# Kernel optimization log

Hardware: AMD Instinct MI355X
Metric: run time of the kernel (lower is better)

Reference implementation:

```python
import jax, jax.numpy as jnp
import numpy as np

HEADS = 8
DIM_HEAD = 64
SCALE = DIM_HEAD ** -0.5
QUERY_DIM = 512
CTX_DIM = 64
INNER = HEADS * DIM_HEAD  # 512
GATE_HID = 32


def setup_inputs() -> dict:
    key = jax.random.key(0)
    ks = jax.random.split(key, 11)
    B, N, M = 4, 2048, 2048
    s = lambda fan: 1.0 / np.sqrt(fan)
    return {
        "x": jax.random.normal(ks[0], (B, N, QUERY_DIM), dtype=jnp.float32),
        "context": jax.random.normal(ks[1], (B, M, CTX_DIM), dtype=jnp.float32),
        "Wq": jax.random.normal(ks[2], (QUERY_DIM, INNER), dtype=jnp.float32) * s(QUERY_DIM),
        "Wk": jax.random.normal(ks[3], (CTX_DIM, INNER), dtype=jnp.float32) * s(CTX_DIM),
        "Wv": jax.random.normal(ks[4], (CTX_DIM, INNER), dtype=jnp.float32) * s(CTX_DIM),
        "W1": jax.random.normal(ks[5], (CTX_DIM, GATE_HID), dtype=jnp.float32) * s(CTX_DIM),
        "b1": jnp.zeros((GATE_HID,), dtype=jnp.float32),
        "W2": jax.random.normal(ks[6], (GATE_HID, 1), dtype=jnp.float32) * s(GATE_HID),
        "b2": jnp.zeros((1,), dtype=jnp.float32),
        "Wo": jax.random.normal(ks[7], (INNER, QUERY_DIM), dtype=jnp.float32) * s(INNER),
        "bo": jnp.zeros((QUERY_DIM,), dtype=jnp.float32),
    }


def reference(x, context, Wq, Wk, Wv, W1, b1, W2, b2, Wo, bo):
    B, N, _ = x.shape
    M = context.shape[1]
    # visual reliability gate: sigmoid(relu(ctx @ W1 + b1) @ W2 + b2) -> [B, M, 1]
    gate = jax.nn.sigmoid(jax.nn.relu(context @ W1 + b1) @ W2 + b2)
    ctx = context * gate
    # projections
    q = (x @ Wq).reshape(B, N, HEADS, DIM_HEAD).transpose(0, 2, 1, 3)    # [B,H,N,D]
    k = (ctx @ Wk).reshape(B, M, HEADS, DIM_HEAD).transpose(0, 2, 1, 3)  # [B,H,M,D]
    v = (ctx @ Wv).reshape(B, M, HEADS, DIM_HEAD).transpose(0, 2, 1, 3)  # [B,H,M,D]
    # scaled dot-product attention (full score matrix, as in source)
    sim = jnp.einsum('bhid,bhjd->bhij', q, k) * SCALE
    attn = jax.nn.softmax(sim, axis=-1)
    out = jnp.einsum('bhij,bhjd->bhid', attn, v)
    out = out.transpose(0, 2, 1, 3).reshape(B, N, INNER)
    return out @ Wo + bo
```

## Files before the change

kernel.cpp:

```cpp
#include <hip/hip_runtime.h>

typedef unsigned short u16;
typedef unsigned int u32;
using frag16 = __attribute__((ext_vector_type(8))) short;
using facc   = __attribute__((ext_vector_type(4))) float;
using facc16 = __attribute__((ext_vector_type(16))) float;

#define DEV static __device__ __forceinline__

DEV u16 f2bf(float f) {
  union { float f; unsigned u; } v; v.f = f;
  unsigned r = v.u + 0x7fffu + ((v.u >> 16) & 1u);
  return (u16)(r >> 16);
}
DEV unsigned fbits(float f) {
  union { float f; unsigned u; } v; v.f = f;
  return v.u;
}
DEV unsigned pkbf(float lo, float hi) {
  return __builtin_amdgcn_perm(fbits(hi) + 0x8000u, fbits(lo) + 0x8000u, 0x07060302u);
}
DEV unsigned pkbf_t(float lo, float hi) {
  return __builtin_amdgcn_perm(fbits(hi), fbits(lo), 0x07060302u);
}
DEV void gld16(const u16* g, u16* l) {
  __builtin_amdgcn_global_load_lds(
      (__attribute__((address_space(1))) unsigned int*)(g),
      (__attribute__((address_space(3))) unsigned int*)(l), 16, 0, 0);
}

__global__ __launch_bounds__(256) void prep_gate_kernel(const float4* __restrict__ x,
    const float* __restrict__ Wq, const float* __restrict__ Wk,
    const float* __restrict__ Wv, const float* __restrict__ Wo,
    const float* __restrict__ ctx, const float* __restrict__ W1,
    const float* __restrict__ b1, const float* __restrict__ W2,
    const float* __restrict__ b2,
    u16* __restrict__ xb, u16* __restrict__ WqT, u16* __restrict__ WkT,
    u16* __restrict__ WvT, u16* __restrict__ WoT, u16* __restrict__ gctx) {
  int bid = blockIdx.x;
  if (bid < 1024) {
    int id = bid * 256 + threadIdx.x;
    const float4* xp = x + (size_t)id * 4;
    u16* op = xb + (size_t)id * 16;
    #pragma unroll
    for (int j = 0; j < 4; ++j) {
      float4 v = xp[j];
      ushort4 o;
      o.x = f2bf(v.x); o.y = f2bf(v.y); o.z = f2bf(v.z); o.w = f2bf(v.w);
      *(ushort4*)(op + j * 4) = o;
    }
  } else if (bid < 1168) {
    int job = bid - 1024;
    const float* W; u16* WT; int K, tile;
    if (job < 64)      { W = Wq; WT = WqT; K = 512; tile = job; }
    else if (job < 72) { W = Wk; WT = WkT; K = 64;  tile = job - 64; }
    else if (job < 80) { W = Wv; WT = WvT; K = 64;  tile = job - 72; }
    else               { W = Wo; WT = WoT; K = 512; tile = job - 80; }
    int tilesK = K >> 6;
    int tr = tile % tilesK, tc = tile / tilesK;
    __shared__ float tl[64][65];
    int c = threadIdx.x & 63, r4 = threadIdx.x >> 6;
    #pragma unroll
    for (int it = 0; it < 16; ++it) {
      int kk = it * 4 + r4;
      tl[kk][c] = W[(size_t)(tr * 64 + kk) * 512 + tc * 64 + c];
    }
    __syncthreads();
    #pragma unroll
    for (int it = 0; it < 16; ++it) {
      int nn = it * 4 + r4;
      WT[(size_t)(tc * 64 + nn) * K + tr * 64 + c] = f2bf(tl[c][nn]);
    }
  } else {
    int wave = threadIdx.x >> 6, lane = threadIdx.x & 63;
    int hi = lane >> 5, hl = lane & 31;
    int row = (bid - 1168) * 4 + wave;
    __shared__ float sc[4][64];
    float cv = ctx[(size_t)row * 64 + lane];
    sc[wave][lane] = cv;
    __syncthreads();
    float hp = 0.f;
    #pragma unroll
    for (int i = 0; i < 32; ++i) {
      int ii = hi * 32 + i;
      hp += sc[wave][ii] * W1[ii * 32 + hl];
    }
    hp += __shfl_xor(hp, 32);
    float hr = fmaxf(hp + b1[hl], 0.f) * W2[hl];
    #pragma unroll
    for (int off = 16; off; off >>= 1) hr += __shfl_xor(hr, off);
    float g = 1.f / (1.f + __expf(-(hr + b2[0])));
    gctx[(size_t)row * 64 + lane] = f2bf(cv * g);
  }
}

template<int MODE>
DEV void gemm128_body(const u16* __restrict__ A, const u16* __restrict__ BT,
                      void* __restrict__ Cp, const float* __restrict__ bias,
                      int m0, int n0, float scale,
                      u16* As, u16* Bs) {
  const int K = 512, N = 512;
  const int lane = threadIdx.x & 63, wave = threadIdx.x >> 6;
  const int quad = lane >> 4, l16 = lane & 15;
  const int wr = wave >> 1, wc = wave & 1;

  const int sr  = lane >> 3;
  const int sc8 = ((lane & 7) ^ sr) * 8;
  const u16* gA = A + (size_t)(m0 + wave * 32 + sr) * K + sc8;
  const u16* gB = BT + (size_t)(n0 + wave * 16 + sr) * K + sc8;

  auto STAGE = [&](int k0, int buf) {
    u16* dA = As + buf * 8192 + wave * 2048;
    #pragma unroll
    for (int j = 0; j < 4; ++j)
      gld16(gA + k0 + (size_t)(j * 8) * K, dA + j * 512);
    u16* dB = Bs + buf * 4096 + wave * 1024;
    #pragma unroll
    for (int j = 0; j < 2; ++j)
      gld16(gB + k0 + (size_t)(j * 8) * K, dB + j * 512);
  };

  facc acc[4][2] = {};
  STAGE(0, 0);
  int buf = 0;
  for (int k0 = 0; k0 < K; k0 += 64) {
    asm volatile("s_waitcnt vmcnt(0)" ::: "memory");
    __builtin_amdgcn_s_barrier();
    if (k0 + 64 < K) STAGE(k0 + 64, buf ^ 1);
    const u16* Ah = As + buf * 8192;
    const u16* Bh = Bs + buf * 4096;
    #pragma unroll
    for (int hh = 0; hh < 2; ++hh) {
      frag16 af[4], bfr[2];
      #pragma unroll
      for (int rt = 0; rt < 4; ++rt) {
        int row = wr * 64 + rt * 16 + l16;
        int ch = (hh * 4 + quad) ^ (row & 7);
        af[rt] = *(const frag16*)(Ah + row * 64 + ch * 8);
      }
      #pragma unroll
      for (int ct = 0; ct < 2; ++ct) {
        int row = wc * 32 + ct * 16 + l16;
        int ch = (hh * 4 + quad) ^ (row & 7);
        bfr[ct] = *(const frag16*)(Bh + row * 64 + ch * 8);
      }
      #pragma unroll
      for (int rt = 0; rt < 4; ++rt)
        #pragma unroll
        for (int ct = 0; ct < 2; ++ct)
          acc[rt][ct] = __builtin_amdgcn_mfma_f32_16x16x32_bf16(af[rt], bfr[ct], acc[rt][ct], 0, 0, 0);
    }
    buf ^= 1;
  }

  #pragma unroll
  for (int rt = 0; rt < 4; ++rt) {
    #pragma unroll
    for (int ct = 0; ct < 2; ++ct) {
      int col = n0 + wc * 32 + ct * 16 + l16;
      int r0g = m0 + wr * 64 + rt * 16 + quad * 4;
      if (MODE == 0) {
        u16* C = (u16*)Cp;
        #pragma unroll
        for (int r = 0; r < 4; ++r)
          C[(size_t)(r0g + r) * N + col] = f2bf(acc[rt][ct][r] * scale);
      } else {
        float* C = (float*)Cp;
        float bv = bias[col];
        #pragma unroll
        for (int r = 0; r < 4; ++r)
          C[(size_t)(r0g + r) * N + col] = acc[rt][ct][r] + bv;
      }
    }
  }
}

__global__ __launch_bounds__(256) void proj_kernel(const u16* __restrict__ xb,
    const u16* __restrict__ WqT, u16* __restrict__ qb,
    const u16* __restrict__ gctx, const u16* __restrict__ BkT,
    const u16* __restrict__ BvT, u16* __restrict__ Kp, u16* __restrict__ Vp) {
  __shared__ __align__(16) u16 As[2 * 128 * 64];
  __shared__ __align__(16) u16 Bs[2 * 64 * 64];
  int bid = blockIdx.x;
  if (bid < 512) {
    int n0 = (bid & 7) * 64, m0 = (bid >> 3) * 128;
    gemm128_body<0>(xb, WqT, qb, nullptr, m0, n0,
                    0.125f * 1.4426950408889634f, As, Bs);
    return;
  }
  bid -= 512;
  const int Kd = 64;
  int lane = threadIdx.x & 63, wave = threadIdx.x >> 6;
  int quad = lane >> 4, l16 = lane & 15;
  int wr = wave >> 1, wc = wave & 1;
  int rowBase = (bid >> 3) * 64 + wr * 32;
  int colBase = (bid & 7) * 64 + wc * 32;
  facc ak[2][2] = {}, av[2][2] = {};
  const u16* a0 = gctx + (size_t)(rowBase + l16) * Kd + quad * 8;
  const u16* a1 = a0 + (size_t)16 * Kd;
  const u16* bk0 = BkT + (size_t)(colBase + l16) * Kd + quad * 8;
  const u16* bk1 = bk0 + (size_t)16 * Kd;
  const u16* bv0 = BvT + (size_t)(colBase + l16) * Kd + quad * 8;
  const u16* bv1 = bv0 + (size_t)16 * Kd;
  #pragma unroll
  for (int kk = 0; kk < Kd; kk += 32) {
    frag16 af0 = *(const frag16*)(a0 + kk);
    frag16 af1 = *(const frag16*)(a1 + kk);
    frag16 k0 = *(const frag16*)(bk0 + kk);
    frag16 k1 = *(const frag16*)(bk1 + kk);
    frag16 v0 = *(const frag16*)(bv0 + kk);
    frag16 v1 = *(const frag16*)(bv1 + kk);
    ak[0][0] = __builtin_amdgcn_mfma_f32_16x16x32_bf16(af0, k0, ak[0][0], 0, 0, 0);
    ak[0][1] = __builtin_amdgcn_mfma_f32_16x16x32_bf16(af0, k1, ak[0][1], 0, 0, 0);
    ak[1][0] = __builtin_amdgcn_mfma_f32_16x16x32_bf16(af1, k0, ak[1][0], 0, 0, 0);
    ak[1][1] = __builtin_amdgcn_mfma_f32_16x16x32_bf16(af1, k1, ak[1][1], 0, 0, 0);
    av[0][0] = __builtin_amdgcn_mfma_f32_16x16x32_bf16(af0, v0, av[0][0], 0, 0, 0);
    av[0][1] = __builtin_amdgcn_mfma_f32_16x16x32_bf16(af0, v1, av[0][1], 0, 0, 0);
    av[1][0] = __builtin_amdgcn_mfma_f32_16x16x32_bf16(af1, v0, av[1][0], 0, 0, 0);
    av[1][1] = __builtin_amdgcn_mfma_f32_16x16x32_bf16(af1, v1, av[1][1], 0, 0, 0);
  }
  #pragma unroll
  for (int rt = 0; rt < 2; ++rt) {
    #pragma unroll
    for (int ct = 0; ct < 2; ++ct) {
      int col = colBase + ct * 16 + l16;
      int r0g = rowBase + rt * 16 + quad * 4;
      int hh = col >> 6, d = col & 63;
      int b = r0g >> 11;
      #pragma unroll
      for (int r = 0; r < 4; ++r) {
        int m = (r0g + r) & 2047;
        size_t addr = ((((size_t)(b * 8 + hh) * 64 + (m >> 5)) * 4 + (d >> 4)) * 64
                       + ((d >> 3) & 1) * 32 + (m & 31)) * 8 + (d & 7);
        Kp[addr] = f2bf(ak[rt][ct][r]);
      }
      int m = r0g & 2047;
      size_t addr = ((((size_t)(b * 8 + hh) * 64 + (m >> 5)) * 4
                      + ((m >> 4) & 1) * 2 + (d >> 5)) * 64
                     + ((m >> 3) & 1) * 32 + (d & 31)) * 8 + (m & 7);
      ushort4 o;
      o.x = f2bf(av[rt][ct][0]); o.y = f2bf(av[rt][ct][1]);
      o.z = f2bf(av[rt][ct][2]); o.w = f2bf(av[rt][ct][3]);
      *(ushort4*)(Vp + addr) = o;
    }
  }
}

__global__ __launch_bounds__(256, 2) void attn_kernel(
    const u16* __restrict__ qb, const u16* __restrict__ Kp,
    const u16* __restrict__ Vp, u16* __restrict__ ob) {
  const int lane = threadIdx.x & 63, wave = threadIdx.x >> 6;
  const int l32 = lane & 31;
  const int hi = lane >> 5;
  const int bid = blockIdx.x;
  const int bh = bid & 31;
  const int qblk = bid >> 5;
  const int b = bh >> 3, h = bh & 7;
  const int q0 = (qblk * 4 + wave) * 32;
  const int rowg = b * 2048 + q0 + l32;

  __shared__ __align__(16) u16 sK[2][2][2048], sV[2][2][2048];

  const u16* qp = qb + (size_t)rowg * 512 + h * 64 + hi * 8;
  frag16 qf0 = *(const frag16*)(qp);
  frag16 qf1 = *(const frag16*)(qp + 16);
  frag16 qf2 = *(const frag16*)(qp + 32);
  frag16 qf3 = *(const frag16*)(qp + 48);

  frag16 ones;
  #pragma unroll
  for (int i = 0; i < 8; ++i) ones[i] = (short)0x3F80;

  facc16 O0 = {}, O1 = {}, Lacc = {};

  const size_t ts = 2048;
  const u16* kpb = Kp + (size_t)(bh * 64) * ts + wave * 512 + lane * 8;
  const u16* vpb = Vp + (size_t)(bh * 64) * ts + wave * 512 + lane * 8;

  gld16(kpb,      sK[0][0] + wave * 512);
  gld16(kpb + ts, sK[0][1] + wave * 512);
  gld16(vpb,      sV[0][0] + wave * 512);
  gld16(vpb + ts, sV[0][1] + wave * 512);

  for (int g = 0; g < 32; ++g) {
    const int p = g & 1;
    __syncthreads();
    if (g + 1 < 32) {
      const size_t t2 = (size_t)(2 * g + 2) * ts;
      gld16(kpb + t2,      sK[p ^ 1][0] + wave * 512);
      gld16(kpb + t2 + ts, sK[p ^ 1][1] + wave * 512);
      gld16(vpb + t2,      sV[p ^ 1][0] + wave * 512);
      gld16(vpb + t2 + ts, sV[p ^ 1][1] + wave * 512);
    }

    frag16 kfa[4], kfb[4];
    #pragma unroll
    for (int i = 0; i < 4; ++i) {
      kfa[i] = *(const frag16*)(sK[p][0] + i * 512 + lane * 8);
      kfb[i] = *(const frag16*)(sK[p][1] + i * 512 + lane * 8);
    }

    facc16 Sa = {}, Sb = {};
    Sa = __builtin_amdgcn_mfma_f32_32x32x16_bf16(kfa[0], qf0, Sa, 0, 0, 0);
    Sb = __builtin_amdgcn_mfma_f32_32x32x16_bf16(kfb[0], qf0, Sb, 0, 0, 0);
    Sa = __builtin_amdgcn_mfma_f32_32x32x16_bf16(kfa[1], qf1, Sa, 0, 0, 0);
    Sb = __builtin_amdgcn_mfma_f32_32x32x16_bf16(kfb[1], qf1, Sb, 0, 0, 0);
    Sa = __builtin_amdgcn_mfma_f32_32x32x16_bf16(kfa[2], qf2, Sa, 0, 0, 0);
    Sb = __builtin_amdgcn_mfma_f32_32x32x16_bf16(kfb[2], qf2, Sb, 0, 0, 0);
    Sa = __builtin_amdgcn_mfma_f32_32x32x16_bf16(kfa[3], qf3, Sa, 0, 0, 0);
    Sb = __builtin_amdgcn_mfma_f32_32x32x16_bf16(kfb[3], qf3, Sb, 0, 0, 0);

    float ea[16], eb[16];
    #pragma unroll
    for (int r = 0; r < 16; ++r) { ea[r] = __builtin_amdgcn_exp2f(Sa[r]);
                                   eb[r] = __builtin_amdgcn_exp2f(Sb[r]); }

    unsigned pua[2][4], pub[2][4];
    #pragma unroll
    for (int c = 0; c < 2; ++c) {
      {
        const float* ee = ea + c * 8;
        unsigned L0 = pkbf_t(ee[0], ee[1]);
        unsigned L1 = pkbf_t(ee[2], ee[3]);
        unsigned H0 = pkbf_t(ee[4], ee[5]);
        unsigned H1 = pkbf_t(ee[6], ee[7]);
        unsigned Y0 = hi ? L0 : H0;
        unsigned Y1 = hi ? L1 : H1;
        unsigned X0 = (unsigned)__shfl_xor((int)Y0, 32);
        unsigned X1 = (unsigned)__shfl_xor((int)Y1, 32);
        pua[c][0] = hi ? X0 : L0;
        pua[c][1] = hi ? X1 : L1;
        pua[c][2] = hi ? H0 : X0;
        pua[c][3] = hi ? H1 : X1;
      }
      {
        const float* ee = eb + c * 8;
        unsigned L0 = pkbf_t(ee[0], ee[1]);
        unsigned L1 = pkbf_t(ee[2], ee[3]);
        unsigned H0 = pkbf_t(ee[4], ee[5]);
        unsigned H1 = pkbf_t(ee[6], ee[7]);
        unsigned Y0 = hi ? L0 : H0;
        unsigned Y1 = hi ? L1 : H1;
        unsigned X0 = (unsigned)__shfl_xor((int)Y0, 32);
        unsigned X1 = (unsigned)__shfl_xor((int)Y1, 32);
        pub[c][0] = hi ? X0 : L0;
        pub[c][1] = hi ? X1 : L1;
        pub[c][2] = hi ? H0 : X0;
        pub[c][3] = hi ? H1 : X1;
      }
    }
    frag16 Pa0 = *(frag16*)&pua[0][0];
    frag16 Pa1 = *(frag16*)&pua[1][0];
    frag16 Pb0 = *(frag16*)&pub[0][0];
    frag16 Pb1 = *(frag16*)&pub[1][0];

    Lacc = __builtin_amdgcn_mfma_f32_32x32x16_bf16(ones, Pa0, Lacc, 0, 0, 0);
    Lacc = __builtin_amdgcn_mfma_f32_32x32x16_bf16(ones, Pa1, Lacc, 0, 0, 0);
    Lacc = __builtin_amdgcn_mfma_f32_32x32x16_bf16(ones, Pb0, Lacc, 0, 0, 0);
    Lacc = __builtin_amdgcn_mfma_f32_32x32x16_bf16(ones, Pb1, Lacc, 0, 0, 0);

    frag16 vfa[4], vfb[4];
    #pragma unroll
    for (int i = 0; i < 4; ++i) {
      vfa[i] = *(const frag16*)(sV[p][0] + i * 512 + lane * 8);
      vfb[i] = *(const frag16*)(sV[p][1] + i * 512 + lane * 8);
    }

    O0 = __builtin_amdgcn_mfma_f32_32x32x16_bf16(vfa[0], Pa0, O0, 0, 0, 0);
    O1 = __builtin_amdgcn_mfma_f32_32x32x16_bf16(vfa[1], Pa0, O1, 0, 0, 0);
    O0 = __builtin_amdgcn_mfma_f32_32x32x16_bf16(vfa[2], Pa1, O0, 0, 0, 0);
    O1 = __builtin_amdgcn_mfma_f32_32x32x16_bf16(vfa[3], Pa1, O1, 0, 0, 0);
    O0 = __builtin_amdgcn_mfma_f32_32x32x16_bf16(vfb[0], Pb0, O0, 0, 0, 0);
    O1 = __builtin_amdgcn_mfma_f32_32x32x16_bf16(vfb[1], Pb0, O1, 0, 0, 0);
    O0 = __builtin_amdgcn_mfma_f32_32x32x16_bf16(vfb[2], Pb1, O0, 0, 0, 0);
    O1 = __builtin_amdgcn_mfma_f32_32x32x16_bf16(vfb[3], Pb1, O1, 0, 0, 0);
  }

  float rinv = 1.0f / Lacc[0];

  u16* op = ob + (size_t)rowg * 512 + h * 64;
  #pragma unroll
  for (int dt = 0; dt < 2; ++dt) {
    #pragma unroll
    for (int rq = 0; rq < 4; ++rq) {
      float v0, v1, v2, v3;
      if (dt == 0) { v0 = O0[rq*4]; v1 = O0[rq*4+1]; v2 = O0[rq*4+2]; v3 = O0[rq*4+3]; }
      else         { v0 = O1[rq*4]; v1 = O1[rq*4+1]; v2 = O1[rq*4+2]; v3 = O1[rq*4+3]; }
      uint2 pk;
      pk.x = pkbf(v0 * rinv, v1 * rinv);
      pk.y = pkbf(v2 * rinv, v3 * rinv);
      int d0 = dt * 32 + 8 * rq + 4 * hi;
      *(uint2*)(op + d0) = pk;
    }
  }
}

__global__ __launch_bounds__(256) void gemm_out(const u16* __restrict__ A,
    const u16* __restrict__ BT, float* __restrict__ C,
    const float* __restrict__ bias) {
  __shared__ __align__(16) u16 As[2 * 128 * 64];
  __shared__ __align__(16) u16 Bs[2 * 64 * 64];
  int n0 = (blockIdx.x & 7) * 64, m0 = (blockIdx.x >> 3) * 128;
  gemm128_body<2>(A, BT, C, bias, m0, n0, 1.f, As, Bs);
}

extern "C" void kernel_launch(void* const* d_in, const int* in_sizes, int n_in,
                              void* d_out, int out_size, void* d_ws, size_t ws_size,
                              hipStream_t stream) {
  const float* x   = (const float*)d_in[0];
  const float* ctx = (const float*)d_in[1];
  const float* Wq  = (const float*)d_in[2];
  const float* Wk  = (const float*)d_in[3];
  const float* Wv  = (const float*)d_in[4];
  const float* W1  = (const float*)d_in[5];
  const float* b1  = (const float*)d_in[6];
  const float* W2  = (const float*)d_in[7];
  const float* b2  = (const float*)d_in[8];
  const float* Wo  = (const float*)d_in[9];
  const float* bo  = (const float*)d_in[10];
  float* out = (float*)d_out;

  char* ws = (char*)d_ws;
  size_t off = 0;
  auto alloc = [&](size_t bytes) {
    char* p = ws + off;
    off += (bytes + 255) & ~(size_t)255;
    return p;
  };
  u16* xb    = (u16*)alloc(8192ull * 512 * 2);
  u16* qb    = (u16*)alloc(8192ull * 512 * 2);
  u16* Kp    = (u16*)alloc(8192ull * 512 * 2);
  u16* Vp    = (u16*)alloc(8192ull * 512 * 2);
  u16* ob    = (u16*)alloc(8192ull * 512 * 2);
  u16* gctx  = (u16*)alloc(8192ull * 64 * 2);
  u16* WqT   = (u16*)alloc(512ull * 512 * 2);
  u16* WkT   = (u16*)alloc(512ull * 64 * 2);
  u16* WvT   = (u16*)alloc(512ull * 64 * 2);
  u16* WoT   = (u16*)alloc(512ull * 512 * 2);

  prep_gate_kernel<<<3216, 256, 0, stream>>>((const float4*)x, Wq, Wk, Wv, Wo,
                                             ctx, W1, b1, W2, b2,
                                             xb, WqT, WkT, WvT, WoT, gctx);
  proj_kernel<<<1536, 256, 0, stream>>>(xb, WqT, qb, gctx, WkT, WvT, Kp, Vp);
  attn_kernel<<<512, 256, 0, stream>>>(qb, Kp, Vp, ob);
  gemm_out<<<512, 256, 0, stream>>>(ob, WoT, out, bo);
}
```

Before: 167.0 us.

## Split attention KV sequence across wave pairs and merge partial sums in LDS

The attention kernel now gives each block 64 queries instead of 128, with two wave pairs that each process half of the key/value sequence for the same query rows. The grid doubles to 1024 blocks, and partial O and row sums are merged through shared memory at the end. The launch-bounds occupancy hint rises from 2 to 4 blocks. The KV loads lose their double buffering: each iteration loads and then waits behind two barriers, which can expose memory latency.

```diff
diff --git a/kernel.cpp b/kernel.cpp
--- a/kernel.cpp
+++ b/kernel.cpp
@@ -246,17 +246,19 @@
   }
 }
 
-__global__ __launch_bounds__(256, 2) void attn_kernel(
+__global__ __launch_bounds__(256, 4) void attn_kernel(
     const u16* __restrict__ qb, const u16* __restrict__ Kp,
     const u16* __restrict__ Vp, u16* __restrict__ ob) {
   const int lane = threadIdx.x & 63, wave = threadIdx.x >> 6;
+  const int wq = wave & 1;
+  const int ws = wave >> 1;
   const int l32 = lane & 31;
   const int hi = lane >> 5;
   const int bid = blockIdx.x;
   const int bh = bid & 31;
-  const int qblk = bid >> 5;
+  const int qpair = bid >> 5;
   const int b = bh >> 3, h = bh & 7;
-  const int q0 = (qblk * 4 + wave) * 32;
+  const int q0 = qpair * 64 + wq * 32;
   const int rowg = b * 2048 + q0 + l32;
 
   __shared__ __align__(16) u16 sK[2][2][2048], sV[2][2][2048];
@@ -274,30 +276,32 @@
   facc16 O0 = {}, O1 = {}, Lacc = {};
 
   const size_t ts = 2048;
-  const u16* kpb = Kp + (size_t)(bh * 64) * ts + wave * 512 + lane * 8;
-  const u16* vpb = Vp + (size_t)(bh * 64) * ts + wave * 512 + lane * 8;
-
-  gld16(kpb,      sK[0][0] + wave * 512);
-  gld16(kpb + ts, sK[0][1] + wave * 512);
-  gld16(vpb,      sV[0][0] + wave * 512);
-  gld16(vpb + ts, sV[0][1] + wave * 512);
-
-  for (int g = 0; g < 32; ++g) {
-    const int p = g & 1;
+  const u16* kpb = Kp + (size_t)(bh * 64 + ws * 32) * ts + wq * 1024 + lane * 8;
+  const u16* vpb = Vp + (size_t)(bh * 64 + ws * 32) * ts + wq * 1024 + lane * 8;
+
+  auto STAGE = [&](int g) {
+    const size_t t2 = (size_t)(2 * g) * ts;
+    gld16(kpb + t2,            &sK[ws][0][0] + wq * 1024);
+    gld16(kpb + t2 + 512,      &sK[ws][0][0] + wq * 1024 + 512);
+    gld16(kpb + t2 + ts,       &sK[ws][1][0] + wq * 1024);
+    gld16(kpb + t2 + ts + 512, &sK[ws][1][0] + wq * 1024 + 512);
+    gld16(vpb + t2,            &sV[ws][0][0] + wq * 1024);
+    gld16(vpb + t2 + 512,      &sV[ws][0][0] + wq * 1024 + 512);
+    gld16(vpb + t2 + ts,       &sV[ws][1][0] + wq * 1024);
+    gld16(vpb + t2 + ts + 512, &sV[ws][1][0] + wq * 1024 + 512);
+  };
+
+  #pragma unroll 1
+  for (int g = 0; g < 16; ++g) {
     __syncthreads();
-    if (g + 1 < 32) {
-      const size_t t2 = (size_t)(2 * g + 2) * ts;
-      gld16(kpb + t2,      sK[p ^ 1][0] + wave * 512);
-      gld16(kpb + t2 + ts, sK[p ^ 1][1] + wave * 512);
-      gld16(vpb + t2,      sV[p ^ 1][0] + wave * 512);
-      gld16(vpb + t2 + ts, sV[p ^ 1][1] + wave * 512);
-    }
+    STAGE(g);
+    __syncthreads();
 
     frag16 kfa[4], kfb[4];
     #pragma unroll
     for (int i = 0; i < 4; ++i) {
-      kfa[i] = *(const frag16*)(sK[p][0] + i * 512 + lane * 8);
-      kfb[i] = *(const frag16*)(sK[p][1] + i * 512 + lane * 8);
+      kfa[i] = *(const frag16*)(&sK[ws][0][0] + i * 512 + lane * 8);
+      kfb[i] = *(const frag16*)(&sK[ws][1][0] + i * 512 + lane * 8);
     }
 
     facc16 Sa = {}, Sb = {};
@@ -362,8 +366,8 @@
     frag16 vfa[4], vfb[4];
     #pragma unroll
     for (int i = 0; i < 4; ++i) {
-      vfa[i] = *(const frag16*)(sV[p][0] + i * 512 + lane * 8);
-      vfb[i] = *(const frag16*)(sV[p][1] + i * 512 + lane * 8);
+      vfa[i] = *(const frag16*)(&sV[ws][0][0] + i * 512 + lane * 8);
+      vfb[i] = *(const frag16*)(&sV[ws][1][0] + i * 512 + lane * 8);
     }
 
     O0 = __builtin_amdgcn_mfma_f32_32x32x16_bf16(vfa[0], Pa0, O0, 0, 0, 0);
@@ -376,21 +380,40 @@
     O1 = __builtin_amdgcn_mfma_f32_32x32x16_bf16(vfb[3], Pb1, O1, 0, 0, 0);
   }
 
-  float rinv = 1.0f / Lacc[0];
-
-  u16* op = ob + (size_t)rowg * 512 + h * 64;
-  #pragma unroll
-  for (int dt = 0; dt < 2; ++dt) {
-    #pragma unroll
-    for (int rq = 0; rq < 4; ++rq) {
-      float v0, v1, v2, v3;
-      if (dt == 0) { v0 = O0[rq*4]; v1 = O0[rq*4+1]; v2 = O0[rq*4+2]; v3 = O0[rq*4+3]; }
-      else         { v0 = O1[rq*4]; v1 = O1[rq*4+1]; v2 = O1[rq*4+2]; v3 = O1[rq*4+3]; }
-      uint2 pk;
-      pk.x = pkbf(v0 * rinv, v1 * rinv);
-      pk.y = pkbf(v2 * rinv, v3 * rinv);
-      int d0 = dt * 32 + 8 * rq + 4 * hi;
-      *(uint2*)(op + d0) = pk;
+  float* mO = (float*)&sK[0][0][0];
+  float* mL = (float*)&sV[0][0][0];
+  __syncthreads();
+  if (ws == 1) {
+    #pragma unroll
+    for (int r = 0; r < 16; ++r) {
+      mO[r * 128 + wq * 64 + lane]        = O0[r];
+      mO[(r + 16) * 128 + wq * 64 + lane] = O1[r];
+    }
+    mL[wq * 64 + lane] = Lacc[0];
+  }
+  __syncthreads();
+  if (ws == 0) {
+    #pragma unroll
+    for (int r = 0; r < 16; ++r) {
+      O0[r] += mO[r * 128 + wq * 64 + lane];
+      O1[r] += mO[(r + 16) * 128 + wq * 64 + lane];
+    }
+    float rinv = 1.0f / (Lacc[0] + mL[wq * 64 + lane]);
+
+    u16* op = ob + (size_t)rowg * 512 + h * 64;
+    #pragma unroll
+    for (int dt = 0; dt < 2; ++dt) {
+      #pragma unroll
+      for (int rq = 0; rq < 4; ++rq) {
+        float v0e, v1e, v2e, v3e;
+        if (dt == 0) { v0e = O0[rq*4]; v1e = O0[rq*4+1]; v2e = O0[rq*4+2]; v3e = O0[rq*4+3]; }
+        else         { v0e = O1[rq*4]; v1e = O1[rq*4+1]; v2e = O1[rq*4+2]; v3e = O1[rq*4+3]; }
+        uint2 pk;
+        pk.x = pkbf(v0e * rinv, v1e * rinv);
+        pk.y = pkbf(v2e * rinv, v3e * rinv);
+        int d0 = dt * 32 + 8 * rq + 4 * hi;
+        *(uint2*)(op + d0) = pk;
+      }
     }
   }
 }
@@ -442,6 +465,6 @@
                                              ctx, W1, b1, W2, b2,
                                              xb, WqT, WkT, WvT, WoT, gctx);
   proj_kernel<<<1536, 256, 0, stream>>>(xb, WqT, qb, gctx, WkT, WvT, Kp, Vp);
-  attn_kernel<<<512, 256, 0, stream>>>(qb, Kp, Vp, ob);
+  attn_kernel<<<1024, 256, 0, stream>>>(qb, Kp, Vp, ob);
   gemm_out<<<512, 256, 0, stream>>>(ob, WoT, out, bo);
 }
```

After: 168.8 us. No clear change (+1.0%).
